# Kernel optimization log

Hardware: AMD Instinct MI355X
Metric: run time of the kernel (lower is better)

The kernel has to match this reference:

```python
import jax, jax.numpy as jnp
import numpy as np

EMBED_DIM = 768
NUM_HEADS = 12
EPS = 1e-6


def setup_inputs() -> dict:
    key = jax.random.key(0)
    ks = jax.random.split(key, 9)
    B, C, H, W = 8, EMBED_DIM, 48, 48
    std = 0.02
    E = EMBED_DIM
    return {
        "query": jax.random.normal(ks[0], (B, C, H, W), dtype=jnp.float32),
        "Wq": jax.random.normal(ks[1], (E, E), dtype=jnp.float32) * std,
        "bq": jnp.zeros((E,), dtype=jnp.float32),
        "Wk": jax.random.normal(ks[2], (E, E), dtype=jnp.float32) * std,
        "bk": jnp.zeros((E,), dtype=jnp.float32),
        "Wv": jax.random.normal(ks[3], (E, E), dtype=jnp.float32) * std,
        "bv": jnp.zeros((E,), dtype=jnp.float32),
        "Wo": jax.random.normal(ks[4], (E, E), dtype=jnp.float32) * std,
        "bo": jnp.zeros((E,), dtype=jnp.float32),
    }


def reference(query, Wq, bq, Wk, bk, Wv, bv, Wo, bo):
    # query: (B, C, H, W) -> (L, B, E) with L = H*W
    B, C, H, W = query.shape
    L = H * W
    E = C
    h = NUM_HEADS
    d = E // h
    x = query.reshape(B, C, L).transpose(2, 0, 1)  # (L, B, E)

    # cos/sin positional reweighting: pi/2 * (i+1) / L
    idx = (jnp.pi / 2) * jnp.arange(1, L + 1, dtype=x.dtype) / L
    sin = jnp.sin(idx)[None, :, None]  # (1, L, 1)
    cos = jnp.cos(idx)[None, :, None]

    # projections + relu feature map
    q = jax.nn.relu(x @ Wq.T + bq)
    k = jax.nn.relu(x @ Wk.T + bk)
    v = x @ Wv.T + bv

    def to_heads(t):  # (L, B, E) -> (B*h, L, d)
        return t.reshape(L, B * h, d).transpose(1, 0, 2)

    q, k, v = to_heads(q), to_heads(k), to_heads(v)

    q_ = jnp.concatenate([q * sin, q * cos], axis=-1)  # (n, L, 2d)
    k_ = jnp.concatenate([k * sin, k * cos], axis=-1)

    # non-causal linear attention
    kv = jnp.einsum("nld,nlm->ndm", k_, v)              # (n, 2d, d)
    z = 1.0 / jnp.maximum(jnp.einsum("nld,nd->nl", q_, k_.sum(axis=1)), EPS)
    out = jnp.einsum("nld,ndm,nl->nlm", q_, kv, z)       # (n, L, d)

    # residual (DropPath is identity at inference)
    attn = x + out.transpose(1, 0, 2).reshape(L, B, E)
    return attn @ Wo.T + bo
```

## Files before the change

### kernel.cpp

```cpp
#include <hip/hip_runtime.h>


#define L_SEQ 2304
#define BATCH 8
#define EDIM 768
#define NHEAD 12
#define DHEAD 64
#define MROWS (L_SEQ * BATCH)

typedef __attribute__((ext_vector_type(8))) short bf16x8_t;
typedef __attribute__((ext_vector_type(4))) float f32x4_t;

__device__ __forceinline__ float b2f(unsigned short u) {
  union { unsigned int i; float f; } x; x.i = ((unsigned int)u) << 16; return x.f;
}
__device__ __forceinline__ unsigned short f2b(float f) {
  union { float f; unsigned int i; } x; x.f = f;
  unsigned int r = x.i + 0x7FFFu + ((x.i >> 16) & 1u);
  return (unsigned short)(r >> 16);
}

#define GLOAD_LDS16(g, l)                                                     \
  __builtin_amdgcn_global_load_lds(                                           \
      (const __attribute__((address_space(1))) unsigned int*)(g),             \
      (__attribute__((address_space(3))) unsigned int*)(l), 16, 0, 0)

__global__ __launch_bounds__(256) void prep(
    const float* __restrict__ q,
    const float* __restrict__ W0, const float* __restrict__ W1,
    const float* __restrict__ W2, const float* __restrict__ W3,
    unsigned short* __restrict__ wbf, unsigned short* __restrict__ xT,
    float* __restrict__ kvz, float2* __restrict__ sct) {
  __shared__ float tile[64][65];
  int bx = blockIdx.x;
  int t = threadIdx.x;
  if (bx < 2304) {
    int y = bx / 576;
    const float* W = (y == 0) ? W0 : (y == 1) ? W1 : (y == 2) ? W2 : W3;
    unsigned short* d = wbf + (size_t)y * EDIM * EDIM;
    int idx = (bx - y * 576) * 256 + t;
    float4 v = *(const float4*)(W + (size_t)idx * 4);
    ushort4 o;
    o.x = f2b(v.x); o.y = f2b(v.y); o.z = f2b(v.z); o.w = f2b(v.w);
    *(ushort4*)(d + (size_t)idx * 4) = o;
  } else if (bx < 5760) {
    int bb = bx - 2304;
    int e0 = (bb % 12) * 64;
    int l0 = ((bb / 12) % 36) * 64;
    int b = bb / 432;
    int li = t & 63, er = t >> 6;
#pragma unroll
    for (int p = 0; p < 16; p++) {
      int eo = er + p * 4;
      tile[eo][li] = q[((size_t)b * EDIM + (e0 + eo)) * L_SEQ + (l0 + li)];
    }
    __syncthreads();
    int ei = t & 63, lr = t >> 6;
#pragma unroll
    for (int p = 0; p < 16; p++) {
      int lo = lr + p * 4;
      xT[((size_t)b * L_SEQ + (l0 + lo)) * EDIM + (e0 + ei)] = f2b(tile[ei][lo]);
    }
  } else if (bx < 6540) {
    int idx = (bx - 5760) * 256 + t;
    *(float4*)(kvz + (size_t)idx * 4) = make_float4(0.f, 0.f, 0.f, 0.f);
  } else {
    int l = (bx - 6540) * 256 + t;
    if (l < L_SEQ) {
      float sv, cv;
      sincosf(1.5707963267948966f * (float)(l + 1) / 2304.0f, &sv, &cv);
      sct[l] = make_float2(sv, cv);
    }
  }
}

#define ALDSO(b_, h_) ((b_) * 8192 + (h_) * 4096)
#define BLDSO(b_, h_) (16384 + (b_) * 8192 + (h_) * 4096)

#define BAR() __builtin_amdgcn_s_barrier()
#define LGKM0() asm volatile("s_waitcnt lgkmcnt(0)")
#define VMW(N) asm volatile("s_waitcnt vmcnt(" #N ")" ::: "memory")

#define STG_A(h_, kt_, LB_)                                                   \
  GLOAD_LDS16(a_sb + (size_t)((h_) * 64) * EDIM + (kt_) * 64, lds + (LB_) + t * 8)
#define STG_B(h_, kt_, LB_)                                                   \
  GLOAD_LDS16(b_sb + (size_t)((h_) * 64) * EDIM + (kt_) * 64, lds + (LB_) + t * 8)

#define DS_A(SET, B_, H_)                                                     \
  _Pragma("unroll") for (int i_ = 0; i_ < 2; i_++)                            \
  _Pragma("unroll") for (int kk_ = 0; kk_ < 2; kk_++)                         \
    SET[i_][kk_] = *(const bf16x8_t*)(lds + ALDSO(B_, H_) +                   \
                                      ((a_base + i_ * 1024 + kk_ * 32) ^ xorv));

#define DS_B(SET, B_, H_)                                                     \
  _Pragma("unroll") for (int kk_ = 0; kk_ < 2; kk_++)                         \
    SET[kk_] = *(const bf16x8_t*)(lds + BLDSO(B_, H_) +                       \
                                  ((b_base + kk_ * 32) ^ xorv));

#define MFMAQ(ASET, BSET, AH, BH)                                             \
  __builtin_amdgcn_s_setprio(1);                                              \
  _Pragma("unroll") for (int i_ = 0; i_ < 2; i_++)                            \
  _Pragma("unroll") for (int kk_ = 0; kk_ < 2; kk_++)                         \
    acc[(AH) * 2 + i_][BH] = __builtin_amdgcn_mfma_f32_16x16x32_bf16(         \
        ASET[i_][kk_], BSET[kk_], acc[(AH) * 2 + i_][BH], 0, 0, 0);           \
  __builtin_amdgcn_s_setprio(0);

template <int MODE>
__global__ __launch_bounds__(512, 4) void gemm256(
    const unsigned short* __restrict__ A,
    const unsigned short* __restrict__ Wall,
    const float* __restrict__ bias0, const float* __restrict__ bias1,
    const float* __restrict__ bias2,
    unsigned short* __restrict__ dst0, unsigned short* __restrict__ dst1,
    unsigned short* __restrict__ dst2,
    float* __restrict__ dstf) {
  extern __shared__ __align__(16) unsigned short lds[];

  const unsigned short* W;
  const float* bias;
  unsigned short* dst = nullptr;
  bool do_relu = false;
  int rowblk, colblk;
  {
    int nwg = (int)gridDim.x;
    int wg = ((int)blockIdx.x & 7) * (nwg >> 3) + ((int)blockIdx.x >> 3);
    if (MODE == 0) {
      rowblk = wg / 18;
      int c = wg - rowblk * 18;
      colblk = c % 6;
      int z = c / 6;
      W = Wall + (size_t)z * EDIM * EDIM;
      bias = (z == 0) ? bias0 : (z == 1) ? bias1 : bias2;
      dst = (z == 0) ? dst0 : (z == 1) ? dst1 : dst2;
      do_relu = (z < 2);
    } else {
      rowblk = wg / 6;
      colblk = wg - rowblk * 6;
      W = Wall;
      bias = bias0;
    }
  }
  const int row0 = rowblk * 128;
  const int col0 = colblk * 128;

  const int t = threadIdx.x;
  const int lane = t & 63;
  const int wave = t >> 6;
  const int wm = wave >> 2;
  const int wn = wave & 3;
  const int mrow = lane & 15;
  const int quad = lane >> 4;

  const int xorv = (mrow & 7) << 3;
  const int a_base = (wm * 32 + mrow) * 64 + quad * 8;
  const int b_base = (wn * 16 + mrow) * 64 + quad * 8;

  const int lr_s = t >> 3;
  const int k0_s = ((((t >> 3) & 7) ^ (t & 7)) << 3);
  const unsigned short* a_sb = A + (size_t)(row0 + lr_s) * EDIM + k0_s;
  const unsigned short* b_sb = W + (size_t)(col0 + lr_s) * EDIM + k0_s;

  f32x4_t acc[4][2] = {};
  bf16x8_t aA[2][2], aB[2][2], bA[2], bB[2];

  STG_A(0, 0, ALDSO(0, 0));
  STG_B(0, 0, BLDSO(0, 0));
  STG_A(1, 0, ALDSO(0, 1));
  STG_B(1, 0, BLDSO(0, 1));
  STG_A(0, 1, ALDSO(1, 0));
  STG_B(0, 1, BLDSO(1, 0));
  VMW(2);
  BAR();

#pragma unroll
  for (int i = 0; i < 6; ++i) {
    const int kt0 = 2 * i, kt1 = 2 * i + 1;
    const bool nxt = (i < 5);
    DS_A(aA, 0, 0);
    DS_B(bA, 0, 0);
    STG_A(1, kt1, ALDSO(1, 1));
    BAR();
    MFMAQ(aA, bA, 0, 0);
    LGKM0();
    BAR();
    DS_B(bB, 0, 1);
    STG_B(1, kt1, BLDSO(1, 1));
    BAR();
    MFMAQ(aA, bB, 0, 1);
    LGKM0();
    BAR();
    DS_A(aB, 0, 1);
    if (nxt) STG_A(0, kt0 + 2, ALDSO(0, 0));
    BAR();
    MFMAQ(aB, bA, 1, 0);
    LGKM0();
    BAR();
    if (nxt) STG_B(0, kt0 + 2, BLDSO(0, 0));
    BAR();
    MFMAQ(aB, bB, 1, 1);
    if (nxt) { VMW(2); } else { VMW(0); }
    BAR();
    DS_A(aA, 1, 0);
    DS_B(bA, 1, 0);
    if (nxt) STG_A(1, kt0 + 2, ALDSO(0, 1));
    BAR();
    MFMAQ(aA, bA, 0, 0);
    LGKM0();
    BAR();
    DS_B(bB, 1, 1);
    if (nxt) STG_B(1, kt0 + 2, BLDSO(0, 1));
    BAR();
    MFMAQ(aA, bB, 0, 1);
    LGKM0();
    BAR();
    DS_A(aB, 1, 1);
    if (nxt) STG_A(0, kt1 + 2, ALDSO(1, 0));
    BAR();
    MFMAQ(aB, bA, 1, 0);
    LGKM0();
    BAR();
    if (nxt) STG_B(0, kt1 + 2, BLDSO(1, 0));
    BAR();
    MFMAQ(aB, bB, 1, 1);
    if (nxt) { VMW(2); } else { VMW(0); }
    BAR();
  }

  const int bb = row0 / L_SEQ;
#pragma unroll
  for (int ti = 0; ti < 4; ti++) {
    int rbase = row0 + (ti >> 1) * 64 + wm * 32 + (ti & 1) * 16 + quad * 4;
#pragma unroll
    for (int tj = 0; tj < 2; tj++) {
      int gc = col0 + tj * 64 + wn * 16 + mrow;
      float bv = bias[gc];
#pragma unroll
      for (int r = 0; r < 4; r++) {
        int gr = rbase + r;
        float v = acc[ti][tj][r] + bv;
        if (MODE == 0) {
          if (do_relu) v = fmaxf(v, 0.0f);
          int ll = gr - bb * L_SEQ;
          int n = bb * NHEAD + (gc >> 6);
          dst[((size_t)n * L_SEQ + ll) * DHEAD + (gc & 63)] = f2b(v);
        } else {
          dstf[(size_t)gr * EDIM + gc] = v;
        }
      }
    }
  }
}

__global__ __launch_bounds__(256) void kv_mfma(
    const unsigned short* __restrict__ kbuf, const unsigned short* __restrict__ vbuf,
    const float2* __restrict__ sct,
    float* __restrict__ kvT, float* __restrict__ ksum) {
  constexpr int ST = 40;
  __shared__ __align__(16) unsigned short ksT[128 * ST];
  __shared__ __align__(16) unsigned short vsT[64 * ST];
  __shared__ float ksum_l[128];
  int n = blockIdx.x;
  int lbase = blockIdx.y * 288;
  int t = threadIdx.x;
  int lane = t & 63, wave = t >> 6;
  int mrow = lane & 15, quad = lane >> 4;

  if (t < 128) ksum_l[t] = 0.f;

  int lrd = t >> 3;
  int oct = t & 7;
  int col2 = (lrd + ((oct & 3) << 3)) & 31;
  const unsigned short* kbase = kbuf + (size_t)n * L_SEQ * DHEAD + oct * 8;
  const unsigned short* vbase = vbuf + (size_t)n * L_SEQ * DHEAD + oct * 8;

  int rv = wave * 16 + mrow;
  const unsigned short* vrd = vsT + rv * ST + (((quad + (rv >> 3)) & 3) << 3);

  f32x4_t acc[8] = {};
  float sks[8] = {}, skc[8] = {};

  for (int s = 0; s < 9; s++) {
    int l = lbase + s * 32 + lrd;
    float2 sc = sct[l];
    union { uint4 q; unsigned short u[8]; } kq, vq;
    kq.q = *(const uint4*)(kbase + (size_t)l * DHEAD);
    vq.q = *(const uint4*)(vbase + (size_t)l * DHEAD);
    __syncthreads();
#pragma unroll
    for (int e = 0; e < 8; e++) {
      int d = oct * 8 + e;
      float kval = b2f(kq.u[e]);
      float a = kval * sc.x, c = kval * sc.y;
      ksT[d * ST + col2] = f2b(a);
      ksT[(64 + d) * ST + col2] = f2b(c);
      vsT[d * ST + col2] = vq.u[e];
      sks[e] += a;
      skc[e] += c;
    }
    __syncthreads();
    bf16x8_t af = *(const bf16x8_t*)(vrd);
#pragma unroll
    for (int jt = 0; jt < 8; jt++) {
      int rk = jt * 16 + mrow;
      bf16x8_t bfk = *(const bf16x8_t*)(ksT + rk * ST + (((quad + (rk >> 3)) & 3) << 3));
      acc[jt] = __builtin_amdgcn_mfma_f32_16x16x32_bf16(af, bfk, acc[jt], 0, 0, 0);
    }
  }

#pragma unroll
  for (int e = 0; e < 8; e++) {
    atomicAdd(&ksum_l[oct * 8 + e], sks[e]);
    atomicAdd(&ksum_l[64 + oct * 8 + e], skc[e]);
  }
  __syncthreads();
  if (t < 128) atomicAdd(&ksum[n * 128 + t], ksum_l[t]);

#pragma unroll
  for (int jt = 0; jt < 8; jt++) {
#pragma unroll
    for (int r = 0; r < 4; r++) {
      int m = wave * 16 + quad * 4 + r;
      int j = jt * 16 + mrow;
      atomicAdd(&kvT[((size_t)n * 64 + m) * 128 + j], acc[jt][r]);
    }
  }
}

__global__ __launch_bounds__(256) void attn_mfma(
    const unsigned short* __restrict__ qbuf, const float* __restrict__ kvT,
    const float* __restrict__ ksum, const unsigned short* __restrict__ xT,
    const float2* __restrict__ sct,
    unsigned short* __restrict__ attn) {
  __shared__ __align__(16) unsigned short As[128 * 72];
  __shared__ __align__(16) unsigned short Bs[64 * 136];
  __shared__ float ks_l[128];
  __shared__ float zs[128], zc[128];
  int l0 = blockIdx.x * 128;
  int n = blockIdx.y;
  int t = threadIdx.x;
  int lane = t & 63, wave = t >> 6;
  int mrow = lane & 15, quad = lane >> 4;
  int b = n / NHEAD, hd = n % NHEAD;

  {
    int row = t >> 1, off = (t & 1) * 32;
    const unsigned short* src = qbuf + ((size_t)n * L_SEQ + l0 + row) * DHEAD + off;
    unsigned short* d = As + row * 72 + off;
#pragma unroll
    for (int c = 0; c < 4; c++)
      *(uint4*)(d + c * 8) = *(const uint4*)(src + c * 8);
  }
  {
    int m = t >> 2, part = t & 3;
    const float* src = kvT + ((size_t)n * 64 + m) * 128 + part * 32;
    unsigned short* dBs = Bs + m * 136 + part * 32;
#pragma unroll
    for (int c = 0; c < 4; c++) {
      float4 a = *(const float4*)(src + c * 8);
      float4 bq = *(const float4*)(src + c * 8 + 4);
      ushort4 o1, o2;
      o1.x = f2b(a.x); o1.y = f2b(a.y); o1.z = f2b(a.z); o1.w = f2b(a.w);
      o2.x = f2b(bq.x); o2.y = f2b(bq.y); o2.z = f2b(bq.z); o2.w = f2b(bq.w);
      *(ushort4*)(dBs + c * 8) = o1;
      *(ushort4*)(dBs + c * 8 + 4) = o2;
    }
  }
  if (t < 128) ks_l[t] = ksum[n * 128 + t];
  __syncthreads();

  if (t < 128) {
    float d0 = 0.f, d1 = 0.f;
    const unsigned short* arow = As + t * 72;
#pragma unroll
    for (int j = 0; j < 8; j++) {
      bf16x8_t v = *(const bf16x8_t*)(arow + j * 8);
#pragma unroll
      for (int e = 0; e < 8; e++) {
        float qv = b2f((unsigned short)v[e]);
        d0 += qv * ks_l[j * 8 + e];
        d1 += qv * ks_l[64 + j * 8 + e];
      }
    }
    float2 sc = sct[l0 + t];
    float z = 1.0f / fmaxf(sc.x * d0 + sc.y * d1, 1e-6f);
    zs[t] = z * sc.x;
    zc[t] = z * sc.y;
  }
  __syncthreads();

  int wr = wave * 32;
  f32x4_t acc0[2][4] = {}, acc1[2][4] = {};
#pragma unroll
  for (int ks = 0; ks < 2; ks++) {
    bf16x8_t af[2];
#pragma unroll
    for (int ti = 0; ti < 2; ti++)
      af[ti] = *(const bf16x8_t*)(As + (wr + ti * 16 + mrow) * 72 + ks * 32 + quad * 8);
#pragma unroll
    for (int tj = 0; tj < 4; tj++) {
      bf16x8_t b0 = *(const bf16x8_t*)(Bs + (tj * 16 + mrow) * 136 + ks * 32 + quad * 8);
      bf16x8_t b1 = *(const bf16x8_t*)(Bs + (tj * 16 + mrow) * 136 + 64 + ks * 32 + quad * 8);
#pragma unroll
      for (int ti = 0; ti < 2; ti++) {
        acc0[ti][tj] = __builtin_amdgcn_mfma_f32_16x16x32_bf16(af[ti], b0, acc0[ti][tj], 0, 0, 0);
        acc1[ti][tj] = __builtin_amdgcn_mfma_f32_16x16x32_bf16(af[ti], b1, acc1[ti][tj], 0, 0, 0);
      }
    }
  }

#pragma unroll
  for (int ti = 0; ti < 2; ti++) {
#pragma unroll
    for (int tj = 0; tj < 4; tj++) {
      int m = tj * 16 + mrow;
#pragma unroll
      for (int r = 0; r < 4; r++) {
        int row = wr + ti * 16 + quad * 4 + r;
        int l = l0 + row;
        float ov = zs[row] * acc0[ti][tj][r] + zc[row] * acc1[ti][tj][r];
        float xv = b2f(xT[((size_t)b * L_SEQ + l) * EDIM + hd * DHEAD + m]);
        attn[((size_t)l * BATCH + b) * EDIM + hd * DHEAD + m] = f2b(xv + ov);
      }
    }
  }
}

extern "C" void kernel_launch(void* const* d_in, const int* in_sizes, int n_in,
                              void* d_out, int out_size, void* d_ws, size_t ws_size,
                              hipStream_t stream) {
  const float* query = (const float*)d_in[0];
  const float* Wq = (const float*)d_in[1];
  const float* bq = (const float*)d_in[2];
  const float* Wk = (const float*)d_in[3];
  const float* bk = (const float*)d_in[4];
  const float* Wv = (const float*)d_in[5];
  const float* bv = (const float*)d_in[6];
  const float* Wo = (const float*)d_in[7];
  const float* bo = (const float*)d_in[8];
  float* out = (float*)d_out;

  unsigned short* xT = (unsigned short*)d_out;

  char* ws = (char*)d_ws;
  const size_t SZ = (size_t)MROWS * EDIM * 2;
  unsigned short* qbuf = (unsigned short*)(ws);
  unsigned short* kbuf = (unsigned short*)(ws + SZ);
  unsigned short* vbuf = (unsigned short*)(ws + 2 * SZ);
  unsigned short* attn = kbuf;
  float* kvT  = (float*)(ws + 3 * SZ);
  float* ksum = (float*)(ws + 3 * SZ + 3145728);
  unsigned short* wbf = (unsigned short*)(ws + 3 * SZ + 3145728 + 49152);

  float2* sct = (float2*)((char*)d_out + SZ);

  static bool attr_done = false;
  if (!attr_done) {
    (void)hipFuncSetAttribute((const void*)gemm256<0>,
                              hipFuncAttributeMaxDynamicSharedMemorySize, 65536);
    (void)hipFuncSetAttribute((const void*)gemm256<1>,
                              hipFuncAttributeMaxDynamicSharedMemorySize, 65536);
    attr_done = true;
  }

  prep<<<dim3(6549), 256, 0, stream>>>(query, Wq, Wk, Wv, Wo, wbf, xT, kvT, sct);

  gemm256<0><<<dim3(2592), dim3(512), 65536, stream>>>(
      xT, wbf, bq, bk, bv, qbuf, kbuf, vbuf, nullptr);

  kv_mfma<<<dim3(96, 8), 256, 0, stream>>>(kbuf, vbuf, sct, kvT, ksum);

  attn_mfma<<<dim3(L_SEQ / 128, 96), 256, 0, stream>>>(qbuf, kvT, ksum, xT, sct, attn);

  gemm256<1><<<dim3(864), dim3(512), 65536, stream>>>(
      attn, wbf + 3 * (size_t)EDIM * EDIM, bo, nullptr, nullptr,
      nullptr, nullptr, nullptr, out);
}
```

Measured before the change: 300.2 us.

## Simplify GEMM main loop to one-barrier-per-k-tile double-buffered schedule

Replaces the fine-grained 8-phase ping-pong schedule, with a barrier after every MFMA quarter, by a plain double-buffered loop. Each k-tile loads all A/B fragments from LDS, issues the global-to-LDS prefetch for tile i+2, then runs all 16 MFMAs. This cuts the number of barriers and waitcnts per k-tile. In exchange it loses the interleaving of LDS reads with MFMAs, and the fragment registers grow.

After: 307.2 us. 1.02x slower.

```diff
diff --git a/kernel.cpp b/kernel.cpp
--- a/kernel.cpp
+++ b/kernel.cpp
@@ -74,35 +74,41 @@
   }
 }
 
-#define ALDSO(b_, h_) ((b_) * 8192 + (h_) * 4096)
-#define BLDSO(b_, h_) (16384 + (b_) * 8192 + (h_) * 4096)
+#define ABUF(b_) ((b_) * 8192)
+#define BBUF(b_) (16384 + (b_) * 8192)
 
 #define BAR() __builtin_amdgcn_s_barrier()
+#define SB0() __builtin_amdgcn_sched_barrier(0)
 #define LGKM0() asm volatile("s_waitcnt lgkmcnt(0)")
 #define VMW(N) asm volatile("s_waitcnt vmcnt(" #N ")" ::: "memory")
 
-#define STG_A(h_, kt_, LB_)                                                   \
-  GLOAD_LDS16(a_sb + (size_t)((h_) * 64) * EDIM + (kt_) * 64, lds + (LB_) + t * 8)
-#define STG_B(h_, kt_, LB_)                                                   \
-  GLOAD_LDS16(b_sb + (size_t)((h_) * 64) * EDIM + (kt_) * 64, lds + (LB_) + t * 8)
-
-#define DS_A(SET, B_, H_)                                                     \
-  _Pragma("unroll") for (int i_ = 0; i_ < 2; i_++)                            \
+#define STG_AB(kt_, B_)                                                       \
+  {                                                                           \
+    GLOAD_LDS16(a_sb + (size_t)(kt_) * 64, lds + ABUF(B_) + t * 8);           \
+    GLOAD_LDS16(a_sb + (size_t)64 * EDIM + (size_t)(kt_) * 64,                \
+                lds + ABUF(B_) + 4096 + t * 8);                               \
+    GLOAD_LDS16(b_sb + (size_t)(kt_) * 64, lds + BBUF(B_) + t * 8);           \
+    GLOAD_LDS16(b_sb + (size_t)64 * EDIM + (size_t)(kt_) * 64,                \
+                lds + BBUF(B_) + 4096 + t * 8);                               \
+  }
+
+#define DS_RD(B_)                                                             \
+  _Pragma("unroll") for (int m_ = 0; m_ < 4; m_++)                            \
   _Pragma("unroll") for (int kk_ = 0; kk_ < 2; kk_++)                         \
-    SET[i_][kk_] = *(const bf16x8_t*)(lds + ALDSO(B_, H_) +                   \
-                                      ((a_base + i_ * 1024 + kk_ * 32) ^ xorv));
-
-#define DS_B(SET, B_, H_)                                                     \
+    aF[m_][kk_] = *(const bf16x8_t*)(lds + ABUF(B_) +                         \
+        ((a_base + (m_ >> 1) * 4096 + (m_ & 1) * 1024 + kk_ * 32) ^ xorv));   \
+  _Pragma("unroll") for (int n_ = 0; n_ < 2; n_++)                            \
   _Pragma("unroll") for (int kk_ = 0; kk_ < 2; kk_++)                         \
-    SET[kk_] = *(const bf16x8_t*)(lds + BLDSO(B_, H_) +                       \
-                                  ((b_base + kk_ * 32) ^ xorv));
-
-#define MFMAQ(ASET, BSET, AH, BH)                                             \
+    bF[n_][kk_] = *(const bf16x8_t*)(lds + BBUF(B_) +                         \
+        ((b_base + n_ * 4096 + kk_ * 32) ^ xorv));
+
+#define MFMA16()                                                              \
   __builtin_amdgcn_s_setprio(1);                                              \
-  _Pragma("unroll") for (int i_ = 0; i_ < 2; i_++)                            \
+  _Pragma("unroll") for (int m_ = 0; m_ < 4; m_++)                            \
+  _Pragma("unroll") for (int n_ = 0; n_ < 2; n_++)                            \
   _Pragma("unroll") for (int kk_ = 0; kk_ < 2; kk_++)                         \
-    acc[(AH) * 2 + i_][BH] = __builtin_amdgcn_mfma_f32_16x16x32_bf16(         \
-        ASET[i_][kk_], BSET[kk_], acc[(AH) * 2 + i_][BH], 0, 0, 0);           \
+    acc[m_][n_] = __builtin_amdgcn_mfma_f32_16x16x32_bf16(                    \
+        aF[m_][kk_], bF[n_][kk_], acc[m_][n_], 0, 0, 0);                      \
   __builtin_amdgcn_s_setprio(0);
 
 template <int MODE>
@@ -161,68 +167,23 @@
   const unsigned short* b_sb = W + (size_t)(col0 + lr_s) * EDIM + k0_s;
 
   f32x4_t acc[4][2] = {};
-  bf16x8_t aA[2][2], aB[2][2], bA[2], bB[2];
-
-  STG_A(0, 0, ALDSO(0, 0));
-  STG_B(0, 0, BLDSO(0, 0));
-  STG_A(1, 0, ALDSO(0, 1));
-  STG_B(1, 0, BLDSO(0, 1));
-  STG_A(0, 1, ALDSO(1, 0));
-  STG_B(0, 1, BLDSO(1, 0));
-  VMW(2);
+  bf16x8_t aF[4][2], bF[2][2];
+
+  STG_AB(0, 0);
+  STG_AB(1, 1);
+  VMW(4);
   BAR();
 
 #pragma unroll
-  for (int i = 0; i < 6; ++i) {
-    const int kt0 = 2 * i, kt1 = 2 * i + 1;
-    const bool nxt = (i < 5);
-    DS_A(aA, 0, 0);
-    DS_B(bA, 0, 0);
-    STG_A(1, kt1, ALDSO(1, 1));
-    BAR();
-    MFMAQ(aA, bA, 0, 0);
+  for (int i = 0; i < 12; ++i) {
+    const int cur = i & 1;
+    DS_RD(cur);
+    SB0();
     LGKM0();
     BAR();
-    DS_B(bB, 0, 1);
-    STG_B(1, kt1, BLDSO(1, 1));
-    BAR();
-    MFMAQ(aA, bB, 0, 1);
-    LGKM0();
-    BAR();
-    DS_A(aB, 0, 1);
-    if (nxt) STG_A(0, kt0 + 2, ALDSO(0, 0));
-    BAR();
-    MFMAQ(aB, bA, 1, 0);
-    LGKM0();
-    BAR();
-    if (nxt) STG_B(0, kt0 + 2, BLDSO(0, 0));
-    BAR();
-    MFMAQ(aB, bB, 1, 1);
-    if (nxt) { VMW(2); } else { VMW(0); }
-    BAR();
-    DS_A(aA, 1, 0);
-    DS_B(bA, 1, 0);
-    if (nxt) STG_A(1, kt0 + 2, ALDSO(0, 1));
-    BAR();
-    MFMAQ(aA, bA, 0, 0);
-    LGKM0();
-    BAR();
-    DS_B(bB, 1, 1);
-    if (nxt) STG_B(1, kt0 + 2, BLDSO(0, 1));
-    BAR();
-    MFMAQ(aA, bB, 0, 1);
-    LGKM0();
-    BAR();
-    DS_A(aB, 1, 1);
-    if (nxt) STG_A(0, kt1 + 2, ALDSO(1, 0));
-    BAR();
-    MFMAQ(aB, bA, 1, 0);
-    LGKM0();
-    BAR();
-    if (nxt) STG_B(0, kt1 + 2, BLDSO(1, 0));
-    BAR();
-    MFMAQ(aB, bB, 1, 1);
-    if (nxt) { VMW(2); } else { VMW(0); }
+    if (i < 10) STG_AB(i + 2, cur);
+    MFMA16();
+    if (i < 10) { VMW(4); } else { VMW(0); }
     BAR();
   }
 
```
